# Kernel optimization log

Measured on AMD Instinct MI355X. Metric: run time of the kernel, lower is better.

Reference implementation:

```python
import jax, jax.numpy as jnp
import numpy as np

N_ATOMS = 100000
N_EDGES = 1600000
N_FRAGS = 10000
N_FRAG_EDGES = 80000
D = 128


def setup_inputs() -> dict:
    key = jax.random.key(0)
    ks = jax.random.split(key, 16)
    s = 1.0 / np.sqrt(D)
    return {
        "x_atoms": jax.random.normal(ks[0], (N_ATOMS, D), jnp.float32),
        "edge_index": jax.random.randint(ks[1], (2, N_EDGES), 0, N_ATOMS),
        "edge_attr": jax.random.normal(ks[2], (N_EDGES, D), jnp.float32),
        "frag_index": jax.random.randint(ks[3], (2, N_FRAG_EDGES), 0, N_FRAGS),
        "x_frags": jax.random.normal(ks[4], (N_FRAGS, D), jnp.float32),
        "atom_to_frag_ids": jax.random.randint(ks[5], (N_ATOMS,), 0, N_FRAGS),
        # parameters (stored [in, out]); only layers actually used in forward
        "atom_w": jax.random.uniform(ks[6], (D, D), jnp.float32, -s, s),
        "atom_b": jax.random.uniform(ks[7], (D,), jnp.float32, -s, s),
        "edge_w": jax.random.uniform(ks[8], (D, D), jnp.float32, -s, s),
        "edge_b": jax.random.uniform(ks[9], (D,), jnp.float32, -s, s),
        "frag_w1": jax.random.uniform(ks[10], (D, 2 * D), jnp.float32, -s, s),
        "frag_b1": jax.random.uniform(ks[11], (2 * D,), jnp.float32, -s, s),
        "frag_w2": jax.random.uniform(ks[12], (2 * D, D), jnp.float32, -(1.0 / np.sqrt(2 * D)), 1.0 / np.sqrt(2 * D)),
        "frag_b2": jax.random.uniform(ks[13], (D,), jnp.float32, -(1.0 / np.sqrt(2 * D)), 1.0 / np.sqrt(2 * D)),
    }


def reference(x_atoms, edge_index, edge_attr, frag_index, x_frags,
              atom_to_frag_ids, atom_w, atom_b, edge_w, edge_b,
              frag_w1, frag_b1, frag_w2, frag_b2):
    n = x_atoms.shape[0]
    n_frags = x_frags.shape[0]

    # add self loops
    loop = jnp.arange(n, dtype=edge_index.dtype)
    src = jnp.concatenate([edge_index[0], loop])
    tgt = jnp.concatenate([edge_index[1], loop])
    self_loop_attr = jnp.zeros((n, edge_attr.shape[1]), edge_attr.dtype)
    edge_attr_full = jnp.concatenate([edge_attr, self_loop_attr], axis=0)

    # embeddings
    h = x_atoms @ atom_w + atom_b                      # [N, D]
    _e = edge_attr_full @ edge_w + edge_b              # computed but unused (as in source)

    # symmetric degree normalization over source-node degree
    deg = jax.ops.segment_sum(jnp.ones_like(src, dtype=h.dtype), src, num_segments=n)
    dinv = jnp.where(deg > 0, deg ** -0.5, 0.0)
    norm = dinv[src] * dinv[tgt]                       # [E+N]

    # gather - scale - scatter_add
    msg = h[src] * norm[:, None]                       # [E+N, D]
    x_atoms_new = jax.ops.segment_sum(msg, tgt, num_segments=n)

    # pool atoms into fragments
    frag_feats = jax.ops.segment_sum(x_atoms_new, atom_to_frag_ids, num_segments=n_frags)

    # fragment-level message passing
    fsrc, ftgt = frag_index[0], frag_index[1]
    frag_sum = jax.ops.segment_sum(frag_feats[fsrc], ftgt, num_segments=n_frags)

    # frag_mlp: Linear(D, 2D) -> ReLU -> Linear(2D, D)
    x_frags_new = jax.nn.relu(frag_sum @ frag_w1 + frag_b1) @ frag_w2 + frag_b2
    return (x_atoms_new, x_frags_new)
```

## Files before the change

kernel.cpp:

```cpp
#include <hip/hip_runtime.h>

constexpr int DD = 128;

typedef __attribute__((ext_vector_type(8))) short short8_t;
typedef __attribute__((ext_vector_type(4))) float f32x4;

__device__ __forceinline__ float bf2f(unsigned short u) {
  union { unsigned int i; float f; } c;
  c.i = ((unsigned int)u) << 16;
  return c.f;
}
__device__ __forceinline__ unsigned short f2bf(float f) {
  union { float f; unsigned int i; } c;
  c.f = f;
  unsigned int x = c.i;
  x += 0x7fff + ((x >> 16) & 1);
  return (unsigned short)(x >> 16);
}

__global__ void __launch_bounds__(256) counts_k(
    const int* __restrict__ esrc, const int* __restrict__ etgt, int E,
    const int* __restrict__ a2f, int N, const int* __restrict__ ftgt, int FE,
    int* __restrict__ cnt_src, int* __restrict__ cnt_tgt,
    int* __restrict__ cnt_a2f, int* __restrict__ cnt_fe,
    int* __restrict__ rank_tgt, int* __restrict__ rank_a2f, int* __restrict__ rank_fe) {
  int i = blockIdx.x * 256 + threadIdx.x;
  if (i < E) {
    atomicAdd(&cnt_src[esrc[i]], 1);
    rank_tgt[i] = atomicAdd(&cnt_tgt[etgt[i]], 1);
  } else if (i < E + N) {
    int j = i - E;
    rank_a2f[j] = atomicAdd(&cnt_a2f[a2f[j]], 1);
  } else if (i < E + N + FE) {
    int e = i - E - N;
    rank_fe[e] = atomicAdd(&cnt_fe[ftgt[e]], 1);
  }
}

__global__ void __launch_bounds__(1024) bsum1024_k(
    const int* __restrict__ cnt_tgt, int n, int nb, int* __restrict__ bsums,
    const int* __restrict__ cnt_a2f, int* __restrict__ off_a2f,
    const int* __restrict__ cnt_fe, int* __restrict__ off_fe, int nf) {
  __shared__ int s[1024];
  int t = threadIdx.x;
  int bid = blockIdx.x;
  if (bid < nb) {
    int g = bid * 1024 + t;
    s[t] = (g < n) ? cnt_tgt[g] : 0;
    __syncthreads();
    for (int d = 512; d > 0; d >>= 1) {
      if (t < d) s[t] += s[t + d];
      __syncthreads();
    }
    if (t == 0) bsums[bid] = s[0];
  } else {
    const int* in = (bid == nb) ? cnt_a2f : cnt_fe;
    int* off = (bid == nb) ? off_a2f : off_fe;
    int carry = 0;
    for (int base = 0; base < nf; base += 1024) {
      int v = (base + t < nf) ? in[base + t] : 0;
      __syncthreads();
      s[t] = v;
      __syncthreads();
      for (int d = 1; d < 1024; d <<= 1) {
        int u = (t >= d) ? s[t - d] : 0;
        __syncthreads();
        s[t] += u;
        __syncthreads();
      }
      int tot = s[1023];
      if (base + t < nf) off[base + t] = s[t] - v + carry;
      carry += tot;
    }
  }
}

__global__ void __launch_bounds__(256) scanB_k(
    const int* __restrict__ in, int n, const int* __restrict__ bsums,
    int* __restrict__ off, const int* __restrict__ cnt_src,
    float* __restrict__ dinv) {
  __shared__ int s[256];
  int t = threadIdx.x;
  int bid = blockIdx.x;
  s[t] = (t < bid) ? bsums[t] : 0;
  __syncthreads();
  for (int d = 128; d > 0; d >>= 1) {
    if (t < d) s[t] += s[t + d];
    __syncthreads();
  }
  int prefix = s[0];
  __syncthreads();

  int base = bid * 1024 + t * 4;
  int a0 = (base + 0 < n) ? in[base + 0] : 0;
  int a1 = (base + 1 < n) ? in[base + 1] : 0;
  int a2 = (base + 2 < n) ? in[base + 2] : 0;
  int a3 = (base + 3 < n) ? in[base + 3] : 0;
  int tot = a0 + a1 + a2 + a3;
  s[t] = tot;
  __syncthreads();
  for (int d = 1; d < 256; d <<= 1) {
    int u = (t >= d) ? s[t - d] : 0;
    __syncthreads();
    s[t] += u;
    __syncthreads();
  }
  int pre = s[t] - tot + prefix;
  int e0 = pre, e1 = pre + a0, e2 = e1 + a1, e3 = e2 + a2;
  if (base + 0 < n) { off[base + 0] = e0; dinv[base + 0] = rsqrtf((float)(cnt_src[base + 0] + 1)); }
  if (base + 1 < n) { off[base + 1] = e1; dinv[base + 1] = rsqrtf((float)(cnt_src[base + 1] + 1)); }
  if (base + 2 < n) { off[base + 2] = e2; dinv[base + 2] = rsqrtf((float)(cnt_src[base + 2] + 1)); }
  if (base + 3 < n) { off[base + 3] = e3; dinv[base + 3] = rsqrtf((float)(cnt_src[base + 3] + 1)); }
}

__global__ void __launch_bounds__(256) gemm_fill_k(
    const float* __restrict__ x, const float* __restrict__ W,
    const float* __restrict__ bias, const float* __restrict__ dinv,
    unsigned short* __restrict__ hout, int nbg,
    const int* __restrict__ esrc, const int* __restrict__ etgt, int E,
    const int* __restrict__ a2f, int N,
    const int* __restrict__ fsrc, const int* __restrict__ ftgt, int FE,
    const int* __restrict__ off_tgt, const int* __restrict__ rank_tgt,
    const int* __restrict__ off_a2f, const int* __restrict__ rank_a2f,
    const int* __restrict__ off_fe, const int* __restrict__ rank_fe,
    int* __restrict__ csr_src, int* __restrict__ aids, int* __restrict__ csr_fs) {
  __shared__ unsigned int wt[8192];

  if ((int)blockIdx.x >= nbg) {
    int i = ((int)blockIdx.x - nbg) * 256 + threadIdx.x;
    if (i < E) {
      csr_src[off_tgt[etgt[i]] + rank_tgt[i]] = esrc[i];
    } else if (i < E + N) {
      int j = i - E;
      aids[off_a2f[a2f[j]] + rank_a2f[j]] = j;
    } else if (i < E + N + FE) {
      int e = i - E - N;
      csr_fs[off_fe[ftgt[e]] + rank_fe[e]] = fsrc[e];
    }
    return;
  }

  const int tid = threadIdx.x;
  const int rbase = blockIdx.x * 128;

  {
    int c = tid & 127;
    int half = tid >> 7;
#pragma unroll 4
    for (int j = 0; j < 32; j++) {
      int p = j * 2 + half;
      int k = p * 2;
      float w0 = W[k * 128 + c];
      float w1 = W[(k + 1) * 128 + c];
      unsigned int packed = (unsigned int)f2bf(w0) | ((unsigned int)f2bf(w1) << 16);
      wt[(64 * c + p) ^ ((c & 7) << 2)] = packed;
    }
  }

  const int wave = tid >> 6;
  const int lane = tid & 63;
  const int l15 = lane & 15;
  const int kg = lane >> 4;

  float bcol[8];
#pragma unroll
  for (int ct = 0; ct < 8; ct++) bcol[ct] = bias[ct * 16 + l15];
  float dv[8];
#pragma unroll
  for (int rt = 0; rt < 2; rt++)
#pragma unroll
    for (int i = 0; i < 4; i++) {
      int gr = rbase + wave * 32 + rt * 16 + kg * 4 + i;
      dv[rt * 4 + i] = (gr < N) ? dinv[gr] : 0.f;
    }

  __syncthreads();

  f32x4 acc[2][8];
#pragma unroll
  for (int rt = 0; rt < 2; rt++)
#pragma unroll
    for (int ct = 0; ct < 8; ct++) acc[rt][ct] = (f32x4)(0.f);

#pragma unroll
  for (int ks = 0; ks < 4; ks++) {
    int kcol = ks * 32 + kg * 8;
    short8_t a[2];
#pragma unroll
    for (int rt = 0; rt < 2; rt++) {
      int row = rbase + wave * 32 + rt * 16 + l15;
      if (row < N) {
        const float4* xr = reinterpret_cast<const float4*>(x + (size_t)row * 128 + kcol);
        float4 v0 = xr[0], v1 = xr[1];
        a[rt][0] = (short)f2bf(v0.x); a[rt][1] = (short)f2bf(v0.y);
        a[rt][2] = (short)f2bf(v0.z); a[rt][3] = (short)f2bf(v0.w);
        a[rt][4] = (short)f2bf(v1.x); a[rt][5] = (short)f2bf(v1.y);
        a[rt][6] = (short)f2bf(v1.z); a[rt][7] = (short)f2bf(v1.w);
      } else {
#pragma unroll
        for (int e = 0; e < 8; e++) a[rt][e] = 0;
      }
    }
#pragma unroll
    for (int ct = 0; ct < 8; ct++) {
      int col = ct * 16 + l15;
      int dw0 = (64 * col + ks * 16 + kg * 4) ^ ((col & 7) << 2);
      short8_t b = *reinterpret_cast<const short8_t*>(&wt[dw0]);
      acc[0][ct] = __builtin_amdgcn_mfma_f32_16x16x32_bf16(a[0], b, acc[0][ct], 0, 0, 0);
      acc[1][ct] = __builtin_amdgcn_mfma_f32_16x16x32_bf16(a[1], b, acc[1][ct], 0, 0, 0);
    }
  }

#pragma unroll
  for (int rt = 0; rt < 2; rt++)
#pragma unroll
    for (int ct = 0; ct < 8; ct++)
#pragma unroll
      for (int i = 0; i < 4; i++) {
        int gr = rbase + wave * 32 + rt * 16 + kg * 4 + i;
        if (gr < N)
          hout[(size_t)gr * 128 + ct * 16 + l15] =
              f2bf((acc[rt][ct][i] + bcol[ct]) * dv[rt * 4 + i]);
      }
}

template<int IC, int OC, bool RELU, int RPT>
__global__ void __launch_bounds__(256) linear_k(
    const float* __restrict__ in, const float* __restrict__ W,
    const float* __restrict__ bias, float* __restrict__ out, int nrows) {
  constexpr int GROUPS = 256 / OC;
  constexpr int RBLK = RPT * GROUPS;
  __shared__ float xs[RBLK * IC];
  const int tid = threadIdx.x;
  const int c = tid % OC;
  const int g = tid / OC;
  const int rbase = blockIdx.x * RBLK;

  constexpr int NV = RBLK * IC / 4;
  const float4* in4 = reinterpret_cast<const float4*>(in);
  for (int idx = tid; idx < NV; idx += 256) {
    int r = idx / (IC / 4);
    int kk = idx % (IC / 4);
    int gr = rbase + r;
    float4 v = make_float4(0.f, 0.f, 0.f, 0.f);
    if (gr < nrows) v = in4[(size_t)gr * (IC / 4) + kk];
    reinterpret_cast<float4*>(xs)[idx] = v;
  }
  __syncthreads();

  float acc[RPT];
  float b = bias[c];
#pragma unroll
  for (int m = 0; m < RPT; m++) acc[m] = b;

#pragma unroll 4
  for (int k = 0; k < IC; k++) {
    float w = W[k * OC + c];
#pragma unroll
    for (int m = 0; m < RPT; m++)
      acc[m] += xs[(g + m * GROUPS) * IC + k] * w;
  }

#pragma unroll
  for (int m = 0; m < RPT; m++) {
    int gr = rbase + g + m * GROUPS;
    if (gr < nrows) {
      float v = acc[m];
      if (RELU) v = fmaxf(v, 0.f);
      out[(size_t)gr * OC + c] = v;
    }
  }
}

__global__ void __launch_bounds__(256) edge_gather_k(
    const int* __restrict__ off, const int* __restrict__ cnt,
    const int* __restrict__ csr_src, const unsigned short* __restrict__ h,
    const float* __restrict__ dinv, float* __restrict__ out, int n) {
  int tn = blockIdx.x * 8 + (threadIdx.x >> 5);
  if (tn >= n) return;
  int lane = threadIdx.x & 31;
  const ushort4* h4 = reinterpret_cast<const ushort4*>(h);
  ushort4 hv = h4[(size_t)tn * 32 + lane];
  float ax = bf2f(hv.x), ay = bf2f(hv.y), az = bf2f(hv.z), aw = bf2f(hv.w);
  int s0 = off[tn], c = cnt[tn];
  int i = 0;
  for (; i + 4 <= c; i += 4) {
    int s1 = csr_src[s0 + i + 0];
    int s2 = csr_src[s0 + i + 1];
    int s3 = csr_src[s0 + i + 2];
    int s4 = csr_src[s0 + i + 3];
    ushort4 v1 = h4[(size_t)s1 * 32 + lane];
    ushort4 v2 = h4[(size_t)s2 * 32 + lane];
    ushort4 v3 = h4[(size_t)s3 * 32 + lane];
    ushort4 v4 = h4[(size_t)s4 * 32 + lane];
    ax += (bf2f(v1.x) + bf2f(v2.x)) + (bf2f(v3.x) + bf2f(v4.x));
    ay += (bf2f(v1.y) + bf2f(v2.y)) + (bf2f(v3.y) + bf2f(v4.y));
    az += (bf2f(v1.z) + bf2f(v2.z)) + (bf2f(v3.z) + bf2f(v4.z));
    aw += (bf2f(v1.w) + bf2f(v2.w)) + (bf2f(v3.w) + bf2f(v4.w));
  }
  for (; i < c; i++) {
    int s1 = csr_src[s0 + i];
    ushort4 v1 = h4[(size_t)s1 * 32 + lane];
    ax += bf2f(v1.x); ay += bf2f(v1.y); az += bf2f(v1.z); aw += bf2f(v1.w);
  }
  float dt = dinv[tn];
  reinterpret_cast<float4*>(out)[(size_t)tn * 32 + lane] =
      make_float4(ax * dt, ay * dt, az * dt, aw * dt);
}

__global__ void __launch_bounds__(256) seg_gather_k(
    const int* __restrict__ off, const int* __restrict__ cnt,
    const int* __restrict__ ids, const float* __restrict__ src_rows,
    float* __restrict__ dst, int n) {
  int f = blockIdx.x * 8 + (threadIdx.x >> 5);
  if (f >= n) return;
  int lane = threadIdx.x & 31;
  const float4* s4 = reinterpret_cast<const float4*>(src_rows);
  float ax = 0.f, ay = 0.f, az = 0.f, aw = 0.f;
  int s0 = off[f], c = cnt[f];
  int i = 0;
  for (; i + 2 <= c; i += 2) {
    int a1 = ids[s0 + i], a2 = ids[s0 + i + 1];
    float4 v1 = s4[(size_t)a1 * 32 + lane];
    float4 v2 = s4[(size_t)a2 * 32 + lane];
    ax += v1.x + v2.x; ay += v1.y + v2.y; az += v1.z + v2.z; aw += v1.w + v2.w;
  }
  if (i < c) {
    int a1 = ids[s0 + i];
    float4 v1 = s4[(size_t)a1 * 32 + lane];
    ax += v1.x; ay += v1.y; az += v1.z; aw += v1.w;
  }
  reinterpret_cast<float4*>(dst)[(size_t)f * 32 + lane] = make_float4(ax, ay, az, aw);
}

extern "C" void kernel_launch(void* const* d_in, const int* in_sizes, int n_in,
                              void* d_out, int out_size, void* d_ws, size_t ws_size,
                              hipStream_t stream) {
  const float* x_atoms    = (const float*)d_in[0];
  const int*   edge_index = (const int*)d_in[1];
  const int*   frag_index = (const int*)d_in[3];
  const int*   a2f     = (const int*)d_in[5];
  const float* atom_w  = (const float*)d_in[6];
  const float* atom_b  = (const float*)d_in[7];
  const float* frag_w1 = (const float*)d_in[10];
  const float* frag_b1 = (const float*)d_in[11];
  const float* frag_w2 = (const float*)d_in[12];
  const float* frag_b2 = (const float*)d_in[13];

  const int N  = in_sizes[0] / DD;
  const int E  = in_sizes[1] / 2;
  const int FE = in_sizes[3] / 2;
  const int NF = in_sizes[4] / DD;

  const int* esrc = edge_index;
  const int* etgt = edge_index + E;
  const int* fsrc = frag_index;
  const int* ftgt = frag_index + FE;

  float* out_atoms = (float*)d_out;
  float* out_frags = out_atoms + (size_t)N * DD;

  char* ws = (char*)d_ws;
  size_t off_b = 0;
  auto alloc = [&](size_t bytes) {
    void* p = ws + off_b;
    off_b += (bytes + 255) & ~(size_t)255;
    return p;
  };
  unsigned short* h = (unsigned short*)alloc((size_t)N * DD * 2);
  float* dinv     = (float*)alloc((size_t)N * 4);
  int*   cnts     = (int*)alloc(((size_t)2 * N + 2 * NF) * 4);
  int*   cnt_src  = cnts;
  int*   cnt_tgt  = cnts + N;
  int*   cnt_a2f  = cnts + 2 * N;
  int*   cnt_fe   = cnts + 2 * N + NF;
  int*   off_tgt  = (int*)alloc((size_t)N * 4);
  int*   rank_tgt = (int*)alloc((size_t)E * 4);
  int*   csr_src  = (int*)alloc((size_t)E * 4);
  int*   off_a2f  = (int*)alloc((size_t)NF * 4);
  int*   rank_a2f = (int*)alloc((size_t)N * 4);
  int*   aids     = (int*)alloc((size_t)N * 4);
  int*   off_fe   = (int*)alloc((size_t)NF * 4);
  int*   rank_fe  = (int*)alloc((size_t)FE * 4);
  int*   csr_fs   = (int*)alloc((size_t)FE * 4);
  int*   bsums    = (int*)alloc(1024 * 4);
  float* ff       = (float*)alloc((size_t)NF * DD * 4);
  float* fs       = (float*)alloc((size_t)NF * DD * 4);
  float* hid      = (float*)alloc((size_t)NF * 2 * DD * 4);

  hipMemsetAsync(cnts, 0, ((size_t)2 * N + 2 * NF) * 4, stream);

  int nb_cnt = (E + N + FE + 255) / 256;
  counts_k<<<nb_cnt, 256, 0, stream>>>(
      esrc, etgt, E, a2f, N, ftgt, FE,
      cnt_src, cnt_tgt, cnt_a2f, cnt_fe, rank_tgt, rank_a2f, rank_fe);

  int nb1 = (N + 1023) / 1024;
  bsum1024_k<<<nb1 + 2, 1024, 0, stream>>>(cnt_tgt, N, nb1, bsums,
                                           cnt_a2f, off_a2f, cnt_fe, off_fe, NF);
  scanB_k<<<nb1, 256, 0, stream>>>(cnt_tgt, N, bsums, off_tgt, cnt_src, dinv);

  int nb_gemm = (N + 127) / 128;
  gemm_fill_k<<<nb_gemm + nb_cnt, 256, 0, stream>>>(
      x_atoms, atom_w, atom_b, dinv, h, nb_gemm,
      esrc, etgt, E, a2f, N, fsrc, ftgt, FE,
      off_tgt, rank_tgt, off_a2f, rank_a2f, off_fe, rank_fe,
      csr_src, aids, csr_fs);

  edge_gather_k<<<(N + 7) / 8, 256, 0, stream>>>(off_tgt, cnt_tgt, csr_src, h, dinv, out_atoms, N);
  seg_gather_k<<<(NF + 7) / 8, 256, 0, stream>>>(off_a2f, cnt_a2f, aids, out_atoms, ff, NF);
  seg_gather_k<<<(NF + 7) / 8, 256, 0, stream>>>(off_fe, cnt_fe, csr_fs, ff, fs, NF);

  linear_k<128, 256, true, 32><<<(NF + 31) / 32, 256, 0, stream>>>(fs, frag_w1, frag_b1, hid, NF);
  linear_k<256, 128, false, 16><<<(NF + 31) / 32, 256, 0, stream>>>(hid, frag_w2, frag_b2, out_frags, NF);
}
```

Before: 380.2 us.

## Move atom GEMM into counting kernel and apply dinv scaling in fill pass

The atom embedding GEMM moves from the CSR-fill kernel into the edge-counting kernel, so it shares a launch with the atomic counting work and no longer has to wait for the degree scan. The dinv row scaling, which needs the scan result, becomes a separate elementwise pass folded into the fill kernel that reads and rewrites h in bf16. This aims to overlap the GEMM with the atomics, but it adds an extra read and write of h and a second bf16 rounding.

```diff
diff --git a/kernel.cpp b/kernel.cpp
--- a/kernel.cpp
+++ b/kernel.cpp
@@ -3,6 +3,7 @@
 constexpr int DD = 128;
 
 typedef __attribute__((ext_vector_type(8))) short short8_t;
+typedef __attribute__((ext_vector_type(8))) unsigned short ushort8_t;
 typedef __attribute__((ext_vector_type(4))) float f32x4;
 
 __device__ __forceinline__ float bf2f(unsigned short u) {
@@ -18,23 +19,104 @@
   return (unsigned short)(x >> 16);
 }
 
-__global__ void __launch_bounds__(256) counts_k(
+__global__ void __launch_bounds__(256) counts_gemm_k(
+    const float* __restrict__ x, const float* __restrict__ W,
+    const float* __restrict__ bias, unsigned short* __restrict__ hout, int nbg,
     const int* __restrict__ esrc, const int* __restrict__ etgt, int E,
     const int* __restrict__ a2f, int N, const int* __restrict__ ftgt, int FE,
     int* __restrict__ cnt_src, int* __restrict__ cnt_tgt,
     int* __restrict__ cnt_a2f, int* __restrict__ cnt_fe,
     int* __restrict__ rank_tgt, int* __restrict__ rank_a2f, int* __restrict__ rank_fe) {
-  int i = blockIdx.x * 256 + threadIdx.x;
-  if (i < E) {
-    atomicAdd(&cnt_src[esrc[i]], 1);
-    rank_tgt[i] = atomicAdd(&cnt_tgt[etgt[i]], 1);
-  } else if (i < E + N) {
-    int j = i - E;
-    rank_a2f[j] = atomicAdd(&cnt_a2f[a2f[j]], 1);
-  } else if (i < E + N + FE) {
-    int e = i - E - N;
-    rank_fe[e] = atomicAdd(&cnt_fe[ftgt[e]], 1);
-  }
+  __shared__ unsigned int wt[8192];
+
+  if ((int)blockIdx.x >= nbg) {
+    int i = ((int)blockIdx.x - nbg) * 256 + threadIdx.x;
+    if (i < E) {
+      atomicAdd(&cnt_src[esrc[i]], 1);
+      rank_tgt[i] = atomicAdd(&cnt_tgt[etgt[i]], 1);
+    } else if (i < E + N) {
+      int j = i - E;
+      rank_a2f[j] = atomicAdd(&cnt_a2f[a2f[j]], 1);
+    } else if (i < E + N + FE) {
+      int e = i - E - N;
+      rank_fe[e] = atomicAdd(&cnt_fe[ftgt[e]], 1);
+    }
+    return;
+  }
+
+  const int tid = threadIdx.x;
+  const int rbase = blockIdx.x * 128;
+
+  {
+    int c = tid & 127;
+    int half = tid >> 7;
+#pragma unroll 4
+    for (int j = 0; j < 32; j++) {
+      int p = j * 2 + half;
+      int k = p * 2;
+      float w0 = W[k * 128 + c];
+      float w1 = W[(k + 1) * 128 + c];
+      unsigned int packed = (unsigned int)f2bf(w0) | ((unsigned int)f2bf(w1) << 16);
+      wt[(64 * c + p) ^ ((c & 7) << 2)] = packed;
+    }
+  }
+
+  const int wave = tid >> 6;
+  const int lane = tid & 63;
+  const int l15 = lane & 15;
+  const int kg = lane >> 4;
+
+  float bcol[8];
+#pragma unroll
+  for (int ct = 0; ct < 8; ct++) bcol[ct] = bias[ct * 16 + l15];
+
+  __syncthreads();
+
+  f32x4 acc[2][8];
+#pragma unroll
+  for (int rt = 0; rt < 2; rt++)
+#pragma unroll
+    for (int ct = 0; ct < 8; ct++) acc[rt][ct] = (f32x4)(0.f);
+
+#pragma unroll
+  for (int ks = 0; ks < 4; ks++) {
+    int kcol = ks * 32 + kg * 8;
+    short8_t a[2];
+#pragma unroll
+    for (int rt = 0; rt < 2; rt++) {
+      int row = rbase + wave * 32 + rt * 16 + l15;
+      if (row < N) {
+        const float4* xr = reinterpret_cast<const float4*>(x + (size_t)row * 128 + kcol);
+        float4 v0 = xr[0], v1 = xr[1];
+        a[rt][0] = (short)f2bf(v0.x); a[rt][1] = (short)f2bf(v0.y);
+        a[rt][2] = (short)f2bf(v0.z); a[rt][3] = (short)f2bf(v0.w);
+        a[rt][4] = (short)f2bf(v1.x); a[rt][5] = (short)f2bf(v1.y);
+        a[rt][6] = (short)f2bf(v1.z); a[rt][7] = (short)f2bf(v1.w);
+      } else {
+#pragma unroll
+        for (int e = 0; e < 8; e++) a[rt][e] = 0;
+      }
+    }
+#pragma unroll
+    for (int ct = 0; ct < 8; ct++) {
+      int col = ct * 16 + l15;
+      int dw0 = (64 * col + ks * 16 + kg * 4) ^ ((col & 7) << 2);
+      short8_t b = *reinterpret_cast<const short8_t*>(&wt[dw0]);
+      acc[0][ct] = __builtin_amdgcn_mfma_f32_16x16x32_bf16(a[0], b, acc[0][ct], 0, 0, 0);
+      acc[1][ct] = __builtin_amdgcn_mfma_f32_16x16x32_bf16(a[1], b, acc[1][ct], 0, 0, 0);
+    }
+  }
+
+#pragma unroll
+  for (int rt = 0; rt < 2; rt++)
+#pragma unroll
+    for (int ct = 0; ct < 8; ct++)
+#pragma unroll
+      for (int i = 0; i < 4; i++) {
+        int gr = rbase + wave * 32 + rt * 16 + kg * 4 + i;
+        if (gr < N)
+          hout[(size_t)gr * 128 + ct * 16 + l15] = f2bf(acc[rt][ct][i] + bcol[ct]);
+      }
 }
 
 __global__ void __launch_bounds__(1024) bsum1024_k(
@@ -113,115 +195,36 @@
   if (base + 3 < n) { off[base + 3] = e3; dinv[base + 3] = rsqrtf((float)(cnt_src[base + 3] + 1)); }
 }
 
-__global__ void __launch_bounds__(256) gemm_fill_k(
-    const float* __restrict__ x, const float* __restrict__ W,
-    const float* __restrict__ bias, const float* __restrict__ dinv,
-    unsigned short* __restrict__ hout, int nbg,
+__global__ void __launch_bounds__(256) fill_scale_k(
     const int* __restrict__ esrc, const int* __restrict__ etgt, int E,
     const int* __restrict__ a2f, int N,
     const int* __restrict__ fsrc, const int* __restrict__ ftgt, int FE,
     const int* __restrict__ off_tgt, const int* __restrict__ rank_tgt,
     const int* __restrict__ off_a2f, const int* __restrict__ rank_a2f,
     const int* __restrict__ off_fe, const int* __restrict__ rank_fe,
-    int* __restrict__ csr_src, int* __restrict__ aids, int* __restrict__ csr_fs) {
-  __shared__ unsigned int wt[8192];
-
-  if ((int)blockIdx.x >= nbg) {
-    int i = ((int)blockIdx.x - nbg) * 256 + threadIdx.x;
-    if (i < E) {
-      csr_src[off_tgt[etgt[i]] + rank_tgt[i]] = esrc[i];
-    } else if (i < E + N) {
-      int j = i - E;
-      aids[off_a2f[a2f[j]] + rank_a2f[j]] = j;
-    } else if (i < E + N + FE) {
-      int e = i - E - N;
-      csr_fs[off_fe[ftgt[e]] + rank_fe[e]] = fsrc[e];
+    int* __restrict__ csr_src, int* __restrict__ aids, int* __restrict__ csr_fs,
+    unsigned short* __restrict__ h, const float* __restrict__ dinv, int nbf) {
+  if ((int)blockIdx.x >= nbf) {
+    int idx = ((int)blockIdx.x - nbf) * 256 + threadIdx.x;
+    if (idx < N * 16) {
+      float d = dinv[idx >> 4];
+      ushort8_t v = reinterpret_cast<ushort8_t*>(h)[idx];
+#pragma unroll
+      for (int e = 0; e < 8; e++) v[e] = f2bf(bf2f(v[e]) * d);
+      reinterpret_cast<ushort8_t*>(h)[idx] = v;
     }
     return;
   }
-
-  const int tid = threadIdx.x;
-  const int rbase = blockIdx.x * 128;
-
-  {
-    int c = tid & 127;
-    int half = tid >> 7;
-#pragma unroll 4
-    for (int j = 0; j < 32; j++) {
-      int p = j * 2 + half;
-      int k = p * 2;
-      float w0 = W[k * 128 + c];
-      float w1 = W[(k + 1) * 128 + c];
-      unsigned int packed = (unsigned int)f2bf(w0) | ((unsigned int)f2bf(w1) << 16);
-      wt[(64 * c + p) ^ ((c & 7) << 2)] = packed;
-    }
-  }
-
-  const int wave = tid >> 6;
-  const int lane = tid & 63;
-  const int l15 = lane & 15;
-  const int kg = lane >> 4;
-
-  float bcol[8];
-#pragma unroll
-  for (int ct = 0; ct < 8; ct++) bcol[ct] = bias[ct * 16 + l15];
-  float dv[8];
-#pragma unroll
-  for (int rt = 0; rt < 2; rt++)
-#pragma unroll
-    for (int i = 0; i < 4; i++) {
-      int gr = rbase + wave * 32 + rt * 16 + kg * 4 + i;
-      dv[rt * 4 + i] = (gr < N) ? dinv[gr] : 0.f;
-    }
-
-  __syncthreads();
-
-  f32x4 acc[2][8];
-#pragma unroll
-  for (int rt = 0; rt < 2; rt++)
-#pragma unroll
-    for (int ct = 0; ct < 8; ct++) acc[rt][ct] = (f32x4)(0.f);
-
-#pragma unroll
-  for (int ks = 0; ks < 4; ks++) {
-    int kcol = ks * 32 + kg * 8;
-    short8_t a[2];
-#pragma unroll
-    for (int rt = 0; rt < 2; rt++) {
-      int row = rbase + wave * 32 + rt * 16 + l15;
-      if (row < N) {
-        const float4* xr = reinterpret_cast<const float4*>(x + (size_t)row * 128 + kcol);
-        float4 v0 = xr[0], v1 = xr[1];
-        a[rt][0] = (short)f2bf(v0.x); a[rt][1] = (short)f2bf(v0.y);
-        a[rt][2] = (short)f2bf(v0.z); a[rt][3] = (short)f2bf(v0.w);
-        a[rt][4] = (short)f2bf(v1.x); a[rt][5] = (short)f2bf(v1.y);
-        a[rt][6] = (short)f2bf(v1.z); a[rt][7] = (short)f2bf(v1.w);
-      } else {
-#pragma unroll
-        for (int e = 0; e < 8; e++) a[rt][e] = 0;
-      }
-    }
-#pragma unroll
-    for (int ct = 0; ct < 8; ct++) {
-      int col = ct * 16 + l15;
-      int dw0 = (64 * col + ks * 16 + kg * 4) ^ ((col & 7) << 2);
-      short8_t b = *reinterpret_cast<const short8_t*>(&wt[dw0]);
-      acc[0][ct] = __builtin_amdgcn_mfma_f32_16x16x32_bf16(a[0], b, acc[0][ct], 0, 0, 0);
-      acc[1][ct] = __builtin_amdgcn_mfma_f32_16x16x32_bf16(a[1], b, acc[1][ct], 0, 0, 0);
-    }
-  }
-
-#pragma unroll
-  for (int rt = 0; rt < 2; rt++)
-#pragma unroll
-    for (int ct = 0; ct < 8; ct++)
-#pragma unroll
-      for (int i = 0; i < 4; i++) {
-        int gr = rbase + wave * 32 + rt * 16 + kg * 4 + i;
-        if (gr < N)
-          hout[(size_t)gr * 128 + ct * 16 + l15] =
-              f2bf((acc[rt][ct][i] + bcol[ct]) * dv[rt * 4 + i]);
-      }
+  int i = blockIdx.x * 256 + threadIdx.x;
+  if (i < E) {
+    csr_src[off_tgt[etgt[i]] + rank_tgt[i]] = esrc[i];
+  } else if (i < E + N) {
+    int j = i - E;
+    aids[off_a2f[a2f[j]] + rank_a2f[j]] = j;
+  } else if (i < E + N + FE) {
+    int e = i - E - N;
+    csr_fs[off_fe[ftgt[e]] + rank_fe[e]] = fsrc[e];
+  }
 }
 
 template<int IC, int OC, bool RELU, int RPT>
@@ -390,8 +393,10 @@
 
   hipMemsetAsync(cnts, 0, ((size_t)2 * N + 2 * NF) * 4, stream);
 
+  int nb_gemm = (N + 127) / 128;
   int nb_cnt = (E + N + FE + 255) / 256;
-  counts_k<<<nb_cnt, 256, 0, stream>>>(
+  counts_gemm_k<<<nb_gemm + nb_cnt, 256, 0, stream>>>(
+      x_atoms, atom_w, atom_b, h, nb_gemm,
       esrc, etgt, E, a2f, N, ftgt, FE,
       cnt_src, cnt_tgt, cnt_a2f, cnt_fe, rank_tgt, rank_a2f, rank_fe);
 
@@ -400,12 +405,11 @@
                                            cnt_a2f, off_a2f, cnt_fe, off_fe, NF);
   scanB_k<<<nb1, 256, 0, stream>>>(cnt_tgt, N, bsums, off_tgt, cnt_src, dinv);
 
-  int nb_gemm = (N + 127) / 128;
-  gemm_fill_k<<<nb_gemm + nb_cnt, 256, 0, stream>>>(
-      x_atoms, atom_w, atom_b, dinv, h, nb_gemm,
+  int nb_scale = (N * 16 + 255) / 256;
+  fill_scale_k<<<nb_cnt + nb_scale, 256, 0, stream>>>(
       esrc, etgt, E, a2f, N, fsrc, ftgt, FE,
       off_tgt, rank_tgt, off_a2f, rank_a2f, off_fe, rank_fe,
-      csr_src, aids, csr_fs);
+      csr_src, aids, csr_fs, h, dinv, nb_cnt);
 
   edge_gather_k<<<(N + 7) / 8, 256, 0, stream>>>(off_tgt, cnt_tgt, csr_src, h, dinv, out_atoms, N);
   seg_gather_k<<<(NF + 7) / 8, 256, 0, stream>>>(off_a2f, cnt_a2f, aids, out_atoms, ff, NF);
```

Result: no change. 379.8 us (-0.1%).
